# Optimization experiments

Hardware: AMD Instinct MI355X
Metric: run time of the kernel (lower is better)

Reference implementation:

```python
import jax, jax.numpy as jnp
import numpy as np

B, N_L, C, NH = 8, 256, 256, 8
HH, WW = 64, 64
N_C = HH * WW
L = 3  # focal_level
KS = [3, 5, 7]  # focal kernel sizes: focal_factor*k + focal_window
HD = C // NH
SCALE = HD ** -0.5


def _dwconv(x, w, k):
    # x: [B,C,H,W], w: [C,1,k,k] depthwise (groups=C)
    p = k // 2
    return jax.lax.conv_general_dilated(
        x, w, window_strides=(1, 1), padding=[(p, p), (p, p)],
        feature_group_count=C,
        dimension_numbers=('NCHW', 'OIHW', 'NCHW'))


def setup_inputs() -> dict:
    key = jax.random.key(0)
    ks = jax.random.split(key, 16)
    s = 0.02
    inp = {
        'latents': jax.random.normal(ks[0], (B, N_L, C), jnp.float32),
        'context': jax.random.normal(ks[1], (B, N_C, C), jnp.float32),
        'q_w': jax.random.normal(ks[2], (C, C), jnp.float32) * s,
        'k_w': jax.random.normal(ks[3], (C, C), jnp.float32) * s,
        'f_w': jax.random.normal(ks[4], (C + L + 1, C), jnp.float32) * s,
        'f_b': jnp.zeros((C + L + 1,), jnp.float32),
        'h_w': jax.random.normal(ks[5], (C, C), jnp.float32) * s,
        'h_b': jnp.zeros((C,), jnp.float32),
        'fk0': jax.random.normal(ks[6], (C, 1, KS[0], KS[0]), jnp.float32) * s,
        'fk1': jax.random.normal(ks[7], (C, 1, KS[1], KS[1]), jnp.float32) * s,
        'fk2': jax.random.normal(ks[8], (C, 1, KS[2], KS[2]), jnp.float32) * s,
        'proj_w': jax.random.normal(ks[9], (C, C), jnp.float32) * s,
        'proj_b': jnp.zeros((C,), jnp.float32),
        'H': HH,
        'W': WW,
    }
    return inp


def reference(latents, context, q_w, k_w, f_w, f_b, h_w, h_b,
              fk0, fk1, fk2, proj_w, proj_b, H, W):
    gelu = lambda x: jax.nn.gelu(x, approximate=False)
    # attention scores
    q = (latents @ q_w.T).reshape(B, N_L, NH, HD).transpose(0, 2, 1, 3)  # [B,NH,Nl,HD]
    k = (context @ k_w.T).reshape(B, N_C, NH, HD).transpose(0, 2, 1, 3)  # [B,NH,Nc,HD]
    attn = jax.nn.softmax(jnp.einsum('bhnd,bhmd->bhnm', q, k) * SCALE, axis=-1)
    # focal modulation on context
    f_out = context.reshape(B, H, W, C) @ f_w.T + f_b          # [B,H,W,C+L+1]
    f_out = f_out.transpose(0, 3, 1, 2)                        # [B,C+L+1,H,W]
    v_ctx, gates = f_out[:, :C], f_out[:, C:]
    v_ctx_all = jnp.zeros_like(v_ctx)
    for l, fk in enumerate((fk0, fk1, fk2)):
        v_ctx = gelu(_dwconv(v_ctx, fk, KS[l]))
        v_ctx_all = v_ctx_all + v_ctx * gates[:, l:l + 1]
    v_global = gelu(v_ctx.mean(axis=(2, 3), keepdims=True))
    v_ctx_all = v_ctx_all + v_global * gates[:, L:L + 1]
    # 1x1 conv modulator
    v_mod = jnp.einsum('bchw,dc->bdhw', v_ctx_all, h_w) + h_b[None, :, None, None]
    # NOTE: faithful to original -- raw reshape of NCHW tensor (no permute)
    v = v_mod.reshape(B, N_C, NH, HD).transpose(0, 2, 1, 3)    # [B,NH,Nc,HD]
    out = jnp.einsum('bhnm,bhmd->bhnd', attn, v)               # [B,NH,Nl,HD]
    out = out.transpose(0, 2, 1, 3).reshape(B, N_L, C)
    out = out @ proj_w.T + proj_b
    return out, attn
```

## Files before the change

### kernel.cpp

```cpp
#include <hip/hip_runtime.h>
#include <math.h>


namespace {

constexpr float CSCALE = 0.17677669529663688f;

typedef __attribute__((ext_vector_type(8))) __bf16 bf16x8;
typedef __attribute__((ext_vector_type(4))) float f32x4;

__device__ __forceinline__ float gelu_f(float x) {
  return 0.5f * x * (1.0f + erff(x * 0.70710678118654752f));
}

__device__ __forceinline__ unsigned short f2bf(float f) {
  union { float f; unsigned u; } v; v.f = f;
  unsigned r = v.u + 0x7fffu + ((v.u >> 16) & 1u);
  return (unsigned short)(r >> 16);
}

__device__ __forceinline__ float bf2f(unsigned short u) {
  union { unsigned u; float f; } v; v.u = (unsigned)u << 16;
  return v.f;
}

__global__ __launch_bounds__(256) void cast_all(
    const float* __restrict__ ctx, const float* __restrict__ lat,
    const float* __restrict__ qw, const float* __restrict__ kw,
    const float* __restrict__ fw, const float* __restrict__ hww,
    const float* __restrict__ pw,
    unsigned short* ctxb, unsigned short* latb, unsigned short* qwb,
    unsigned short* kwb, unsigned short* fwb, unsigned short* hwb,
    unsigned short* pwb) {
  const int blk = blockIdx.x;
  const float* s; unsigned short* d; int b0, nq;
  if      (blk < 2048) { s = ctx; d = ctxb; b0 = blk;        nq = 2097152; }
  else if (blk < 2176) { s = lat; d = latb; b0 = blk - 2048; nq = 131072; }
  else if (blk < 2192) { s = qw;  d = qwb;  b0 = blk - 2176; nq = 16384; }
  else if (blk < 2208) { s = kw;  d = kwb;  b0 = blk - 2192; nq = 16384; }
  else if (blk < 2225) { s = fw;  d = fwb;  b0 = blk - 2208; nq = 16640; }
  else if (blk < 2241) { s = hww; d = hwb;  b0 = blk - 2225; nq = 16384; }
  else                 { s = pw;  d = pwb;  b0 = blk - 2241; nq = 16384; }
  #pragma unroll
  for (int t = 0; t < 4; ++t) {
    const int q = b0*1024 + t*256 + threadIdx.x;
    if (q < nq) {
      float4 v = ((const float4*)s)[q];
      ushort4 o;
      o.x = f2bf(v.x); o.y = f2bf(v.y); o.z = f2bf(v.z); o.w = f2bf(v.w);
      ((ushort4*)d)[q] = o;
    }
  }
}

__global__ __launch_bounds__(256) void mfma_qk(
    const unsigned short* __restrict__ A, const unsigned short* __restrict__ W,
    unsigned short* __restrict__ out) {
  const int r0 = blockIdx.x * 64, n0 = blockIdx.y * 64;
  const int tid = threadIdx.x, w = tid >> 6, l = tid & 63;
  const int lr = l & 15, lk = l >> 4;
  const int rw = r0 + w*16;
  const unsigned short* ap = A + (size_t)(rw + lr)*256 + lk*8;
  f32x4 acc[4] = {{0.f,0.f,0.f,0.f},{0.f,0.f,0.f,0.f},{0.f,0.f,0.f,0.f},{0.f,0.f,0.f,0.f}};
  #pragma unroll
  for (int k0 = 0; k0 < 256; k0 += 32) {
    bf16x8 a = *reinterpret_cast<const bf16x8*>(ap + k0);
    #pragma unroll
    for (int j = 0; j < 4; ++j) {
      bf16x8 b = *reinterpret_cast<const bf16x8*>(W + (size_t)(n0 + j*16 + lr)*256 + k0 + lk*8);
      acc[j] = __builtin_amdgcn_mfma_f32_16x16x32_bf16(a, b, acc[j], 0, 0, 0);
    }
  }
  #pragma unroll
  for (int j = 0; j < 4; ++j)
    #pragma unroll
    for (int rr = 0; rr < 4; ++rr)
      out[(size_t)(rw + lk*4 + rr)*256 + n0 + j*16 + lr] = f2bf(acc[j][rr]);
}

__global__ __launch_bounds__(256) void mfma_fk(
    const unsigned short* __restrict__ A, const unsigned short* __restrict__ Wk,
    const unsigned short* __restrict__ Wf, const float* __restrict__ fb,
    unsigned short* __restrict__ kout, unsigned short* __restrict__ vctx,
    float* __restrict__ gates) {
  const int r0 = blockIdx.x * 64;
  const bool isk = blockIdx.y < 4;
  const int n0 = (isk ? blockIdx.y : blockIdx.y - 4) * 64;
  const unsigned short* W = isk ? Wk : Wf;
  const int tid = threadIdx.x, w = tid >> 6, l = tid & 63;
  const int lr = l & 15, lk = l >> 4;
  const int rw = r0 + w*16;
  const unsigned short* ap = A + (size_t)(rw + lr)*256 + lk*8;
  f32x4 acc[4] = {{0.f,0.f,0.f,0.f},{0.f,0.f,0.f,0.f},{0.f,0.f,0.f,0.f},{0.f,0.f,0.f,0.f}};
  #pragma unroll
  for (int k0 = 0; k0 < 256; k0 += 32) {
    bf16x8 a = *reinterpret_cast<const bf16x8*>(ap + k0);
    #pragma unroll
    for (int j = 0; j < 4; ++j) {
      const int n = n0 + j*16 + lr;
      bf16x8 b = {};
      if (isk || n < 260)
        b = *reinterpret_cast<const bf16x8*>(W + (size_t)n*256 + k0 + lk*8);
      acc[j] = __builtin_amdgcn_mfma_f32_16x16x32_bf16(a, b, acc[j], 0, 0, 0);
    }
  }
  if (isk) {
    #pragma unroll
    for (int j = 0; j < 4; ++j)
      #pragma unroll
      for (int rr = 0; rr < 4; ++rr)
        kout[(size_t)(rw + lk*4 + rr)*256 + n0 + j*16 + lr] = f2bf(acc[j][rr]);
  } else {
    const int rbase = rw + lk*4;
    const int b = rbase >> 12, hw = rbase & 4095;
    #pragma unroll
    for (int j = 0; j < 4; ++j) {
      const int n = n0 + j*16 + lr;
      if (n >= 260) continue;
      const float bb = fb[n];
      if (n < 256) {
        ushort4 o;
        o.x = f2bf(acc[j][0] + bb); o.y = f2bf(acc[j][1] + bb);
        o.z = f2bf(acc[j][2] + bb); o.w = f2bf(acc[j][3] + bb);
        *(ushort4*)&vctx[((size_t)(b*256 + n))*4096 + hw] = o;
      } else {
        float4 o = make_float4(acc[j][0] + bb, acc[j][1] + bb,
                               acc[j][2] + bb, acc[j][3] + bb);
        *(float4*)&gates[((size_t)(b*4 + (n - 256)))*4096 + hw] = o;
      }
    }
  }
}

__global__ __launch_bounds__(256) void fused_conv(
    const unsigned short* in, const float* __restrict__ wk3,
    const float* __restrict__ wk5, const float* __restrict__ wk7,
    const float* __restrict__ gates, unsigned short* out) {
  constexpr int TW = 70;
  __shared__ float A[TW * TW];
  __shared__ float w3[9];
  __shared__ float w5[25];
  __shared__ float w7[49];
  __shared__ float red[4];
  const int tid = threadIdx.x;
  const int b = blockIdx.x >> 8, c = blockIdx.x & 255;
  if (tid < 9)  w3[tid] = wk3[c*9  + tid];
  else if (tid < 34) w5[tid-9]  = wk5[c*25 + tid-9];
  else if (tid < 83) w7[tid-34] = wk7[c*49 + tid-34];
  const unsigned short* ip = in + (size_t)(b*256 + c) * 4096;
  for (int idx = tid; idx < TW*TW; idx += 256) {
    const int ty = idx / TW, tx = idx - ty*TW;
    const int gy = ty - 3, gx = tx - 3;
    A[idx] = (gy >= 0 && gy < 64 && gx >= 0 && gx < 64) ? bf2f(ip[gy*64 + gx]) : 0.0f;
  }
  __syncthreads();
  const float* g0 = gates + (size_t)(b*4 + 0) * 4096;
  const float* g1 = gates + (size_t)(b*4 + 1) * 4096;
  const float* g2 = gates + (size_t)(b*4 + 2) * 4096;
  const float* g3 = gates + (size_t)(b*4 + 3) * 4096;
  float v[16], acc[16];
  #pragma unroll
  for (int ii = 0; ii < 16; ++ii) {
    const int pix = ii*256 + tid;
    const int y = pix >> 6, x = pix & 63;
    float s = 0.f;
    #pragma unroll
    for (int ky = 0; ky < 3; ++ky)
      #pragma unroll
      for (int kx = 0; kx < 3; ++kx)
        s += w3[ky*3 + kx] * A[(y+2+ky)*TW + (x+2+kx)];
    v[ii] = gelu_f(s);
    acc[ii] = v[ii] * g0[pix];
  }
  __syncthreads();
  #pragma unroll
  for (int ii = 0; ii < 16; ++ii) {
    const int pix = ii*256 + tid;
    A[((pix >> 6) + 3)*TW + (pix & 63) + 3] = v[ii];
  }
  __syncthreads();
  #pragma unroll
  for (int ii = 0; ii < 16; ++ii) {
    const int pix = ii*256 + tid;
    const int y = pix >> 6, x = pix & 63;
    float s = 0.f;
    #pragma unroll
    for (int ky = 0; ky < 5; ++ky)
      #pragma unroll
      for (int kx = 0; kx < 5; ++kx)
        s += w5[ky*5 + kx] * A[(y+1+ky)*TW + (x+1+kx)];
    v[ii] = gelu_f(s);
    acc[ii] += v[ii] * g1[pix];
  }
  __syncthreads();
  #pragma unroll
  for (int ii = 0; ii < 16; ++ii) {
    const int pix = ii*256 + tid;
    A[((pix >> 6) + 3)*TW + (pix & 63) + 3] = v[ii];
  }
  __syncthreads();
  float msum = 0.f;
  #pragma unroll
  for (int ii = 0; ii < 16; ++ii) {
    const int pix = ii*256 + tid;
    const int y = pix >> 6, x = pix & 63;
    float s = 0.f;
    #pragma unroll
    for (int ky = 0; ky < 7; ++ky)
      #pragma unroll
      for (int kx = 0; kx < 7; ++kx)
        s += w7[ky*7 + kx] * A[(y+ky)*TW + (x+kx)];
    v[ii] = gelu_f(s);
    acc[ii] += v[ii] * g2[pix];
    msum += v[ii];
  }
  #pragma unroll
  for (int off = 32; off >= 1; off >>= 1) msum += __shfl_xor(msum, off, 64);
  if ((tid & 63) == 0) red[tid >> 6] = msum;
  __syncthreads();
  const float vg = gelu_f((red[0]+red[1]+red[2]+red[3]) * (1.0f/4096.0f));
  unsigned short* vp = out + (size_t)(b*256 + c) * 4096;
  #pragma unroll
  for (int ii = 0; ii < 16; ++ii) {
    const int pix = ii*256 + tid;
    vp[pix] = f2bf(acc[ii] + vg * g3[pix]);
  }
}

__global__ __launch_bounds__(256) void mfma_h(
    const unsigned short* __restrict__ vall, const unsigned short* __restrict__ hwb,
    const float* __restrict__ hb, unsigned short* __restrict__ vlin) {
  __shared__ unsigned short Bs[64][264];
  __shared__ unsigned short Ts[64][72];
  const int hw0 = blockIdx.x * 64, d0 = blockIdx.y * 64, b = blockIdx.z;
  const int tid = threadIdx.x, w = tid >> 6, l = tid & 63;
  const int lr = l & 15, lk = l >> 4;
  const int cl = tid >> 3, hl = (tid & 7) * 8;
  #pragma unroll
  for (int c0 = 0; c0 < 256; c0 += 32) {
    const unsigned short* sp = vall + (size_t)(b*256 + c0 + cl)*4096 + hw0 + hl;
    ushort4 u0 = *(const ushort4*)sp;
    ushort4 u1 = *(const ushort4*)(sp + 4);
    Bs[hl+0][c0+cl] = u0.x; Bs[hl+1][c0+cl] = u0.y;
    Bs[hl+2][c0+cl] = u0.z; Bs[hl+3][c0+cl] = u0.w;
    Bs[hl+4][c0+cl] = u1.x; Bs[hl+5][c0+cl] = u1.y;
    Bs[hl+6][c0+cl] = u1.z; Bs[hl+7][c0+cl] = u1.w;
  }
  __syncthreads();
  const int dw = d0 + w*16;
  const unsigned short* ap = hwb + (size_t)(dw + lr)*256 + lk*8;
  f32x4 acc[4] = {{0.f,0.f,0.f,0.f},{0.f,0.f,0.f,0.f},{0.f,0.f,0.f,0.f},{0.f,0.f,0.f,0.f}};
  #pragma unroll
  for (int k0 = 0; k0 < 256; k0 += 32) {
    bf16x8 a = *reinterpret_cast<const bf16x8*>(ap + k0);
    #pragma unroll
    for (int j = 0; j < 4; ++j) {
      bf16x8 bv = *reinterpret_cast<const bf16x8*>(&Bs[j*16 + lr][k0 + lk*8]);
      acc[j] = __builtin_amdgcn_mfma_f32_16x16x32_bf16(a, bv, acc[j], 0, 0, 0);
    }
  }
  float hbv[4];
  #pragma unroll
  for (int rr = 0; rr < 4; ++rr) hbv[rr] = hb[dw + lk*4 + rr];
  #pragma unroll
  for (int j = 0; j < 4; ++j)
    #pragma unroll
    for (int rr = 0; rr < 4; ++rr)
      Ts[w*16 + lk*4 + rr][j*16 + lr] = f2bf(acc[j][rr] + hbv[rr]);
  __syncthreads();
  const int q = hw0 >> 8, dim0 = hw0 & 255;
  #pragma unroll
  for (int it = 0; it < 2; ++it) {
    const int dl = it*32 + (tid >> 3);
    const int ch = tid & 7;
    const int m = (d0 + dl)*16 + q;
    uint4 v = *(const uint4*)&Ts[dl][ch*8];
    *(uint4*)&vlin[((size_t)(b*4096 + m))*256 + dim0 + ch*8] = v;
  }
}

__global__ __launch_bounds__(256) void trans_bf(
    const unsigned short* __restrict__ vlin, unsigned short* __restrict__ vt) {
  __shared__ unsigned short T[64][72];
  const int tid = threadIdx.x;
  const int m0 = blockIdx.x * 64, d0 = blockIdx.y * 64, b = blockIdx.z;
  #pragma unroll
  for (int it = 0; it < 2; ++it) {
    const int ml = it*32 + (tid >> 3);
    const int ch = tid & 7;
    uint4 v = *(const uint4*)&vlin[((size_t)(b*4096 + m0 + ml))*256 + d0 + ch*8];
    *(uint4*)&T[ml][ch*8] = v;
  }
  __syncthreads();
  #pragma unroll
  for (int it = 0; it < 2; ++it) {
    const int dl = it*32 + (tid >> 3);
    const int ch = tid & 7;
    unsigned short tmp[8];
    #pragma unroll
    for (int k = 0; k < 8; ++k) tmp[k] = T[ch*8 + k][dl];
    *(uint4*)&vt[((size_t)(b*256 + d0 + dl))*4096 + m0 + ch*8] = *(uint4*)tmp;
  }
}

__global__ __launch_bounds__(256) void attn_pv(
    const unsigned short* __restrict__ qb, const unsigned short* __restrict__ kb,
    const unsigned short* __restrict__ vt, float* __restrict__ attn,
    unsigned short* __restrict__ aout) {
  const int blk = blockIdx.x;
  const int bh = blk & 63, nt = blk >> 6;
  const int b = bh >> 3, h = bh & 7;
  const int tid = threadIdx.x;
  const int w = tid >> 6, l = tid & 63;
  const int lr = l & 15, lk = l >> 4;
  const int n0 = nt * 16;
  __shared__ float rs[4][16];
  __shared__ unsigned short pl[4][16][40];
  __shared__ float ps[4][16][34];
  __shared__ float osum[4][16][32];
  bf16x8 aq = *reinterpret_cast<const bf16x8*>(
      qb + ((size_t)(b*256 + n0 + lr))*256 + h*32 + lk*8);
  const unsigned short* kbase = kb + (size_t)b*4096*256 + h*32 + lk*8;
  float sum[4] = {0.f, 0.f, 0.f, 0.f};
  #pragma unroll 2
  for (int mt = 0; mt < 64; ++mt) {
    const int m0 = w*1024 + mt*16;
    bf16x8 bk = *reinterpret_cast<const bf16x8*>(kbase + (size_t)(m0 + lr)*256);
    f32x4 d = __builtin_amdgcn_mfma_f32_16x16x32_bf16(aq, bk, (f32x4){0.f,0.f,0.f,0.f}, 0, 0, 0);
    #pragma unroll
    for (int r = 0; r < 4; ++r) sum[r] += __expf(d[r] * CSCALE);
  }
  #pragma unroll
  for (int r = 0; r < 4; ++r) {
    #pragma unroll
    for (int m = 1; m < 16; m <<= 1) sum[r] += __shfl_xor(sum[r], m, 64);
  }
  if (lr == 0) {
    #pragma unroll
    for (int r = 0; r < 4; ++r) rs[w][lk*4 + r] = sum[r];
  }
  __syncthreads();
  float invS[4];
  #pragma unroll
  for (int r = 0; r < 4; ++r) {
    const int rowi = lk*4 + r;
    invS[r] = 1.0f / (rs[0][rowi] + rs[1][rowi] + rs[2][rowi] + rs[3][rowi]);
  }
  float* ab = attn + ((size_t)bh*256 + n0) * 4096;
  const unsigned short* vb = vt + ((size_t)(b*256 + h*32))*4096;
  const int fr = l >> 5;
  const int fm = l & 31;
  f32x4 acc0 = {0.f,0.f,0.f,0.f}, acc1 = {0.f,0.f,0.f,0.f};
  for (int mt = 0; mt < 64; ++mt) {
    const int m0 = w*1024 + mt*16;
    bf16x8 bk = *reinterpret_cast<const bf16x8*>(kbase + (size_t)(m0 + lr)*256);
    f32x4 d = __builtin_amdgcn_mfma_f32_16x16x32_bf16(aq, bk, (f32x4){0.f,0.f,0.f,0.f}, 0, 0, 0);
    const int mo = (mt & 1) << 4;
    #pragma unroll
    for (int r = 0; r < 4; ++r) {
      const float p = __expf(d[r] * CSCALE) * invS[r];
      ps[w][lk*4 + r][mo + lr] = p;
      pl[w][lk*4 + r][mo + lr] = f2bf(p);
    }
    if (mt & 1) {
      const int mb = w*1024 + (mt - 1)*16;
      bf16x8 pa = *reinterpret_cast<const bf16x8*>(&pl[w][lr][lk*8]);
      bf16x8 bv0 = *reinterpret_cast<const bf16x8*>(vb + (size_t)lr*4096 + mb + lk*8);
      bf16x8 bv1 = *reinterpret_cast<const bf16x8*>(vb + (size_t)(16 + lr)*4096 + mb + lk*8);
      acc0 = __builtin_amdgcn_mfma_f32_16x16x32_bf16(pa, bv0, acc0, 0, 0, 0);
      acc1 = __builtin_amdgcn_mfma_f32_16x16x32_bf16(pa, bv1, acc1, 0, 0, 0);
      #pragma unroll
      for (int i = 0; i < 8; ++i) {
        const int row = i*2 + fr;
        ab[(size_t)row*4096 + mb + fm] = ps[w][row][fm];
      }
    }
  }
  #pragma unroll
  for (int r = 0; r < 4; ++r) {
    osum[w][lk*4 + r][lr]      = acc0[r];
    osum[w][lk*4 + r][16 + lr] = acc1[r];
  }
  __syncthreads();
  for (int i = tid; i < 512; i += 256) {
    const int n = i >> 5, d = i & 31;
    const float s = osum[0][n][d] + osum[1][n][d] + osum[2][n][d] + osum[3][n][d];
    aout[((size_t)(b*256 + n0 + n))*256 + h*32 + d] = f2bf(s);
  }
}

__global__ __launch_bounds__(256) void mfma_proj(
    const unsigned short* __restrict__ A, const unsigned short* __restrict__ W,
    const float* __restrict__ pb, float* __restrict__ out) {
  const int r0 = blockIdx.x * 64, n0 = blockIdx.y * 64;
  const int tid = threadIdx.x, w = tid >> 6, l = tid & 63;
  const int lr = l & 15, lk = l >> 4;
  const int rw = r0 + w*16;
  const unsigned short* ap = A + (size_t)(rw + lr)*256 + lk*8;
  f32x4 acc[4] = {{0.f,0.f,0.f,0.f},{0.f,0.f,0.f,0.f},{0.f,0.f,0.f,0.f},{0.f,0.f,0.f,0.f}};
  #pragma unroll
  for (int k0 = 0; k0 < 256; k0 += 32) {
    bf16x8 a = *reinterpret_cast<const bf16x8*>(ap + k0);
    #pragma unroll
    for (int j = 0; j < 4; ++j) {
      bf16x8 b = *reinterpret_cast<const bf16x8*>(W + (size_t)(n0 + j*16 + lr)*256 + k0 + lk*8);
      acc[j] = __builtin_amdgcn_mfma_f32_16x16x32_bf16(a, b, acc[j], 0, 0, 0);
    }
  }
  #pragma unroll
  for (int j = 0; j < 4; ++j) {
    const int n = n0 + j*16 + lr;
    const float bb = pb[n];
    #pragma unroll
    for (int rr = 0; rr < 4; ++rr)
      out[(size_t)(rw + lk*4 + rr)*256 + n] = acc[j][rr] + bb;
  }
}

}

extern "C" void kernel_launch(void* const* d_in, const int* in_sizes, int n_in,
                              void* d_out, int out_size, void* d_ws, size_t ws_size,
                              hipStream_t stream) {
  (void)in_sizes; (void)n_in; (void)out_size; (void)ws_size;
  const float* latents = (const float*)d_in[0];
  const float* context = (const float*)d_in[1];
  const float* q_w    = (const float*)d_in[2];
  const float* k_w    = (const float*)d_in[3];
  const float* f_w    = (const float*)d_in[4];
  const float* f_b    = (const float*)d_in[5];
  const float* h_w    = (const float*)d_in[6];
  const float* h_b    = (const float*)d_in[7];
  const float* fk0    = (const float*)d_in[8];
  const float* fk1    = (const float*)d_in[9];
  const float* fk2    = (const float*)d_in[10];
  const float* proj_w = (const float*)d_in[11];
  const float* proj_b = (const float*)d_in[12];

  float* out0 = (float*)d_out;
  float* attn = out0 + (size_t)8*256*256;

  char* w = (char*)d_ws;
  unsigned short* ctx_bf = (unsigned short*)(w + 0x0);
  unsigned short* vcv    = (unsigned short*)(w + 0x1000000);
  unsigned short* k_bf   = (unsigned short*)(w + 0x2100000);
  unsigned short* v_tb   = (unsigned short*)(w + 0x3100000);
  unsigned short* q_bf   = (unsigned short*)(w + 0x4100000);
  unsigned short* lat_bf = (unsigned short*)(w + 0x4200000);
  unsigned short* qw_bf  = (unsigned short*)(w + 0x4300000);
  unsigned short* kw_bf  = (unsigned short*)(w + 0x4340000);
  unsigned short* fw_bf  = (unsigned short*)(w + 0x4380000);
  unsigned short* hw_bf  = (unsigned short*)(w + 0x43C0000);
  unsigned short* pw_bf  = (unsigned short*)(w + 0x4400000);
  float*          gates  = (float*)(w + 0x4440000);
  unsigned short* aout_bf= (unsigned short*)(w + 0x44C0000);
  unsigned short* vlin_bf= (unsigned short*)(w + 0x4600000);

  cast_all<<<2257, 256, 0, stream>>>(context, latents, q_w, k_w, f_w, h_w, proj_w,
                                     ctx_bf, lat_bf, qw_bf, kw_bf, fw_bf, hw_bf, pw_bf);
  mfma_qk  <<<dim3(32, 4),  256, 0, stream>>>(lat_bf, qw_bf, q_bf);
  mfma_fk  <<<dim3(512, 9), 256, 0, stream>>>(ctx_bf, kw_bf, fw_bf, f_b, k_bf, vcv, gates);
  fused_conv<<<2048, 256, 0, stream>>>(vcv, fk0, fk1, fk2, gates, vcv);
  mfma_h   <<<dim3(64, 4, 8), 256, 0, stream>>>(vcv, hw_bf, h_b, vlin_bf);
  trans_bf <<<dim3(64, 4, 8), 256, 0, stream>>>(vlin_bf, v_tb);
  attn_pv  <<<1024, 256, 0, stream>>>(q_bf, k_bf, v_tb, attn, aout_bf);
  mfma_proj<<<dim3(32, 4), 256, 0, stream>>>(aout_bf, pw_bf, proj_b, out0);
}
```

Baseline: 342.4 us.

## Fuse activation casts into GEMMs, widen GEMM N tiles, vectorize attn stores

Removes the separate fp32→bf16 cast pass over context and latents, so the Q/K/F GEMMs now read fp32 activations directly and convert them in registers. Each GEMM block now covers the full N dimension (16 or 17 MFMA tiles), so the A rows are read once instead of once per N tile. mfma_h also computes all 256 output channels per block, reusing the transposed LDS tile. The attention-probability writeout to global memory changes from scalar to float4 stores, with the LDS row padding adjusted to keep alignment. In exchange, the large per-thread accumulator arrays raise register pressure and lower occupancy, and context is now read twice in fp32 (once by the K GEMM and once by the F GEMM).

```diff
diff --git a/kernel.cpp b/kernel.cpp
--- a/kernel.cpp
+++ b/kernel.cpp
@@ -24,23 +24,26 @@
   return v.f;
 }
 
-__global__ __launch_bounds__(256) void cast_all(
-    const float* __restrict__ ctx, const float* __restrict__ lat,
+__device__ __forceinline__ bf16x8 pack8(float4 a, float4 b) {
+  union { unsigned short u[8]; bf16x8 v; } A;
+  A.u[0] = f2bf(a.x); A.u[1] = f2bf(a.y); A.u[2] = f2bf(a.z); A.u[3] = f2bf(a.w);
+  A.u[4] = f2bf(b.x); A.u[5] = f2bf(b.y); A.u[6] = f2bf(b.z); A.u[7] = f2bf(b.w);
+  return A.v;
+}
+
+__global__ __launch_bounds__(256) void cast_w(
     const float* __restrict__ qw, const float* __restrict__ kw,
     const float* __restrict__ fw, const float* __restrict__ hww,
     const float* __restrict__ pw,
-    unsigned short* ctxb, unsigned short* latb, unsigned short* qwb,
-    unsigned short* kwb, unsigned short* fwb, unsigned short* hwb,
-    unsigned short* pwb) {
+    unsigned short* qwb, unsigned short* kwb, unsigned short* fwb,
+    unsigned short* hwb, unsigned short* pwb) {
   const int blk = blockIdx.x;
   const float* s; unsigned short* d; int b0, nq;
-  if      (blk < 2048) { s = ctx; d = ctxb; b0 = blk;        nq = 2097152; }
-  else if (blk < 2176) { s = lat; d = latb; b0 = blk - 2048; nq = 131072; }
-  else if (blk < 2192) { s = qw;  d = qwb;  b0 = blk - 2176; nq = 16384; }
-  else if (blk < 2208) { s = kw;  d = kwb;  b0 = blk - 2192; nq = 16384; }
-  else if (blk < 2225) { s = fw;  d = fwb;  b0 = blk - 2208; nq = 16640; }
-  else if (blk < 2241) { s = hww; d = hwb;  b0 = blk - 2225; nq = 16384; }
-  else                 { s = pw;  d = pwb;  b0 = blk - 2241; nq = 16384; }
+  if      (blk < 16) { s = qw;  d = qwb; b0 = blk;      nq = 16384; }
+  else if (blk < 32) { s = kw;  d = kwb; b0 = blk - 16; nq = 16384; }
+  else if (blk < 49) { s = fw;  d = fwb; b0 = blk - 32; nq = 16640; }
+  else if (blk < 65) { s = hww; d = hwb; b0 = blk - 49; nq = 16384; }
+  else               { s = pw;  d = pwb; b0 = blk - 65; nq = 16384; }
   #pragma unroll
   for (int t = 0; t < 4; ++t) {
     const int q = b0*1024 + t*256 + threadIdx.x;
@@ -53,81 +56,77 @@
   }
 }
 
-__global__ __launch_bounds__(256) void mfma_qk(
-    const unsigned short* __restrict__ A, const unsigned short* __restrict__ W,
+__global__ __launch_bounds__(256) void mfma_proj_rw(
+    const float* __restrict__ A, const unsigned short* __restrict__ W,
     unsigned short* __restrict__ out) {
-  const int r0 = blockIdx.x * 64, n0 = blockIdx.y * 64;
+  const int r0 = blockIdx.x * 64;
   const int tid = threadIdx.x, w = tid >> 6, l = tid & 63;
   const int lr = l & 15, lk = l >> 4;
   const int rw = r0 + w*16;
-  const unsigned short* ap = A + (size_t)(rw + lr)*256 + lk*8;
-  f32x4 acc[4] = {{0.f,0.f,0.f,0.f},{0.f,0.f,0.f,0.f},{0.f,0.f,0.f,0.f},{0.f,0.f,0.f,0.f}};
+  const float* ap = A + (size_t)(rw + lr)*256 + lk*8;
+  f32x4 acc[16];
+  #pragma unroll
+  for (int j = 0; j < 16; ++j) acc[j] = (f32x4){0.f,0.f,0.f,0.f};
   #pragma unroll
   for (int k0 = 0; k0 < 256; k0 += 32) {
-    bf16x8 a = *reinterpret_cast<const bf16x8*>(ap + k0);
-    #pragma unroll
-    for (int j = 0; j < 4; ++j) {
-      bf16x8 b = *reinterpret_cast<const bf16x8*>(W + (size_t)(n0 + j*16 + lr)*256 + k0 + lk*8);
+    float4 c0 = *(const float4*)(ap + k0);
+    float4 c1 = *(const float4*)(ap + k0 + 4);
+    bf16x8 a = pack8(c0, c1);
+    #pragma unroll
+    for (int j = 0; j < 16; ++j) {
+      bf16x8 b = *reinterpret_cast<const bf16x8*>(W + (size_t)(j*16 + lr)*256 + k0 + lk*8);
       acc[j] = __builtin_amdgcn_mfma_f32_16x16x32_bf16(a, b, acc[j], 0, 0, 0);
     }
   }
   #pragma unroll
-  for (int j = 0; j < 4; ++j)
+  for (int j = 0; j < 16; ++j)
     #pragma unroll
     for (int rr = 0; rr < 4; ++rr)
-      out[(size_t)(rw + lk*4 + rr)*256 + n0 + j*16 + lr] = f2bf(acc[j][rr]);
-}
-
-__global__ __launch_bounds__(256) void mfma_fk(
-    const unsigned short* __restrict__ A, const unsigned short* __restrict__ Wk,
-    const unsigned short* __restrict__ Wf, const float* __restrict__ fb,
-    unsigned short* __restrict__ kout, unsigned short* __restrict__ vctx,
+      out[(size_t)(rw + lk*4 + rr)*256 + j*16 + lr] = f2bf(acc[j][rr]);
+}
+
+__global__ __launch_bounds__(256) void mfma_f(
+    const float* __restrict__ A, const unsigned short* __restrict__ W,
+    const float* __restrict__ fb, unsigned short* __restrict__ vctx,
     float* __restrict__ gates) {
   const int r0 = blockIdx.x * 64;
-  const bool isk = blockIdx.y < 4;
-  const int n0 = (isk ? blockIdx.y : blockIdx.y - 4) * 64;
-  const unsigned short* W = isk ? Wk : Wf;
   const int tid = threadIdx.x, w = tid >> 6, l = tid & 63;
   const int lr = l & 15, lk = l >> 4;
   const int rw = r0 + w*16;
-  const unsigned short* ap = A + (size_t)(rw + lr)*256 + lk*8;
-  f32x4 acc[4] = {{0.f,0.f,0.f,0.f},{0.f,0.f,0.f,0.f},{0.f,0.f,0.f,0.f},{0.f,0.f,0.f,0.f}};
+  const float* ap = A + (size_t)(rw + lr)*256 + lk*8;
+  f32x4 acc[17];
+  #pragma unroll
+  for (int j = 0; j < 17; ++j) acc[j] = (f32x4){0.f,0.f,0.f,0.f};
   #pragma unroll
   for (int k0 = 0; k0 < 256; k0 += 32) {
-    bf16x8 a = *reinterpret_cast<const bf16x8*>(ap + k0);
-    #pragma unroll
-    for (int j = 0; j < 4; ++j) {
-      const int n = n0 + j*16 + lr;
+    float4 c0 = *(const float4*)(ap + k0);
+    float4 c1 = *(const float4*)(ap + k0 + 4);
+    bf16x8 a = pack8(c0, c1);
+    #pragma unroll
+    for (int j = 0; j < 17; ++j) {
+      const int n = j*16 + lr;
       bf16x8 b = {};
-      if (isk || n < 260)
+      if (n < 260)
         b = *reinterpret_cast<const bf16x8*>(W + (size_t)n*256 + k0 + lk*8);
       acc[j] = __builtin_amdgcn_mfma_f32_16x16x32_bf16(a, b, acc[j], 0, 0, 0);
     }
   }
-  if (isk) {
-    #pragma unroll
-    for (int j = 0; j < 4; ++j)
-      #pragma unroll
-      for (int rr = 0; rr < 4; ++rr)
-        kout[(size_t)(rw + lk*4 + rr)*256 + n0 + j*16 + lr] = f2bf(acc[j][rr]);
-  } else {
-    const int rbase = rw + lk*4;
-    const int b = rbase >> 12, hw = rbase & 4095;
-    #pragma unroll
-    for (int j = 0; j < 4; ++j) {
-      const int n = n0 + j*16 + lr;
-      if (n >= 260) continue;
-      const float bb = fb[n];
-      if (n < 256) {
-        ushort4 o;
-        o.x = f2bf(acc[j][0] + bb); o.y = f2bf(acc[j][1] + bb);
-        o.z = f2bf(acc[j][2] + bb); o.w = f2bf(acc[j][3] + bb);
-        *(ushort4*)&vctx[((size_t)(b*256 + n))*4096 + hw] = o;
-      } else {
-        float4 o = make_float4(acc[j][0] + bb, acc[j][1] + bb,
-                               acc[j][2] + bb, acc[j][3] + bb);
-        *(float4*)&gates[((size_t)(b*4 + (n - 256)))*4096 + hw] = o;
-      }
+  const int rbase = rw + lk*4;
+  const int b = rbase >> 12, hw = rbase & 4095;
+  #pragma unroll
+  for (int j = 0; j < 17; ++j) {
+    const int n = j*16 + lr;
+    if (n >= 260) continue;
+    const float bb = fb[n];
+    if (n < 256) {
+      ushort4 o;
+      o.x = f2bf(acc[j][0] + bb); o.y = f2bf(acc[j][1] + bb);
+      o.z = f2bf(acc[j][2] + bb); o.w = f2bf(acc[j][3] + bb);
+      *(ushort4*)&vctx[((size_t)(b*256 + n))*4096 + hw] = o;
+    } else {
+      float4 o = make_float4(acc[j][0] + bb, acc[j][1] + bb,
+                             acc[j][2] + bb, acc[j][3] + bb);
+      *(float4*)&gates[((size_t)(b*4 + (n - 256)))*4096 + hw] = o;
     }
   }
 }
@@ -230,9 +229,8 @@
 __global__ __launch_bounds__(256) void mfma_h(
     const unsigned short* __restrict__ vall, const unsigned short* __restrict__ hwb,
     const float* __restrict__ hb, unsigned short* __restrict__ vlin) {
-  __shared__ unsigned short Bs[64][264];
-  __shared__ unsigned short Ts[64][72];
-  const int hw0 = blockIdx.x * 64, d0 = blockIdx.y * 64, b = blockIdx.z;
+  __shared__ unsigned short sh[256 * 72];
+  const int hw0 = blockIdx.x * 64, b = blockIdx.y;
   const int tid = threadIdx.x, w = tid >> 6, l = tid & 63;
   const int lr = l & 15, lk = l >> 4;
   const int cl = tid >> 3, hl = (tid & 7) * 8;
@@ -241,40 +239,53 @@
     const unsigned short* sp = vall + (size_t)(b*256 + c0 + cl)*4096 + hw0 + hl;
     ushort4 u0 = *(const ushort4*)sp;
     ushort4 u1 = *(const ushort4*)(sp + 4);
-    Bs[hl+0][c0+cl] = u0.x; Bs[hl+1][c0+cl] = u0.y;
-    Bs[hl+2][c0+cl] = u0.z; Bs[hl+3][c0+cl] = u0.w;
-    Bs[hl+4][c0+cl] = u1.x; Bs[hl+5][c0+cl] = u1.y;
-    Bs[hl+6][c0+cl] = u1.z; Bs[hl+7][c0+cl] = u1.w;
-  }
-  __syncthreads();
-  const int dw = d0 + w*16;
-  const unsigned short* ap = hwb + (size_t)(dw + lr)*256 + lk*8;
-  f32x4 acc[4] = {{0.f,0.f,0.f,0.f},{0.f,0.f,0.f,0.f},{0.f,0.f,0.f,0.f},{0.f,0.f,0.f,0.f}};
+    sh[(hl+0)*264 + c0+cl] = u0.x; sh[(hl+1)*264 + c0+cl] = u0.y;
+    sh[(hl+2)*264 + c0+cl] = u0.z; sh[(hl+3)*264 + c0+cl] = u0.w;
+    sh[(hl+4)*264 + c0+cl] = u1.x; sh[(hl+5)*264 + c0+cl] = u1.y;
+    sh[(hl+6)*264 + c0+cl] = u1.z; sh[(hl+7)*264 + c0+cl] = u1.w;
+  }
+  __syncthreads();
+  const int dw = w * 64;
+  f32x4 acc[4][4];
+  #pragma unroll
+  for (int j2 = 0; j2 < 4; ++j2)
+    #pragma unroll
+    for (int j = 0; j < 4; ++j) acc[j2][j] = (f32x4){0.f,0.f,0.f,0.f};
   #pragma unroll
   for (int k0 = 0; k0 < 256; k0 += 32) {
-    bf16x8 a = *reinterpret_cast<const bf16x8*>(ap + k0);
+    bf16x8 a[4];
+    #pragma unroll
+    for (int j2 = 0; j2 < 4; ++j2)
+      a[j2] = *reinterpret_cast<const bf16x8*>(hwb + (size_t)(dw + j2*16 + lr)*256 + k0 + lk*8);
     #pragma unroll
     for (int j = 0; j < 4; ++j) {
-      bf16x8 bv = *reinterpret_cast<const bf16x8*>(&Bs[j*16 + lr][k0 + lk*8]);
-      acc[j] = __builtin_amdgcn_mfma_f32_16x16x32_bf16(a, bv, acc[j], 0, 0, 0);
-    }
-  }
-  float hbv[4];
-  #pragma unroll
-  for (int rr = 0; rr < 4; ++rr) hbv[rr] = hb[dw + lk*4 + rr];
-  #pragma unroll
-  for (int j = 0; j < 4; ++j)
-    #pragma unroll
-    for (int rr = 0; rr < 4; ++rr)
-      Ts[w*16 + lk*4 + rr][j*16 + lr] = f2bf(acc[j][rr] + hbv[rr]);
+      bf16x8 bv = *reinterpret_cast<const bf16x8*>(&sh[(j*16 + lr)*264 + k0 + lk*8]);
+      #pragma unroll
+      for (int j2 = 0; j2 < 4; ++j2)
+        acc[j2][j] = __builtin_amdgcn_mfma_f32_16x16x32_bf16(a[j2], bv, acc[j2][j], 0, 0, 0);
+    }
+  }
+  float hbv[4][4];
+  #pragma unroll
+  for (int j2 = 0; j2 < 4; ++j2)
+    #pragma unroll
+    for (int rr = 0; rr < 4; ++rr) hbv[j2][rr] = hb[dw + j2*16 + lk*4 + rr];
+  __syncthreads();
+  #pragma unroll
+  for (int j2 = 0; j2 < 4; ++j2)
+    #pragma unroll
+    for (int j = 0; j < 4; ++j)
+      #pragma unroll
+      for (int rr = 0; rr < 4; ++rr)
+        sh[(dw + j2*16 + lk*4 + rr)*72 + j*16 + lr] = f2bf(acc[j2][j][rr] + hbv[j2][rr]);
   __syncthreads();
   const int q = hw0 >> 8, dim0 = hw0 & 255;
   #pragma unroll
-  for (int it = 0; it < 2; ++it) {
+  for (int it = 0; it < 8; ++it) {
     const int dl = it*32 + (tid >> 3);
     const int ch = tid & 7;
-    const int m = (d0 + dl)*16 + q;
-    uint4 v = *(const uint4*)&Ts[dl][ch*8];
+    const int m = dl*16 + q;
+    uint4 v = *(const uint4*)&sh[dl*72 + ch*8];
     *(uint4*)&vlin[((size_t)(b*4096 + m))*256 + dim0 + ch*8] = v;
   }
 }
@@ -316,7 +327,7 @@
   const int n0 = nt * 16;
   __shared__ float rs[4][16];
   __shared__ unsigned short pl[4][16][40];
-  __shared__ float ps[4][16][34];
+  __shared__ float ps[4][16][36];
   __shared__ float osum[4][16][32];
   bf16x8 aq = *reinterpret_cast<const bf16x8*>(
       qb + ((size_t)(b*256 + n0 + lr))*256 + h*32 + lk*8);
@@ -348,8 +359,8 @@
   }
   float* ab = attn + ((size_t)bh*256 + n0) * 4096;
   const unsigned short* vb = vt + ((size_t)(b*256 + h*32))*4096;
-  const int fr = l >> 5;
-  const int fm = l & 31;
+  const int fr = l >> 3;
+  const int fm = (l & 7) * 4;
   f32x4 acc0 = {0.f,0.f,0.f,0.f}, acc1 = {0.f,0.f,0.f,0.f};
   for (int mt = 0; mt < 64; ++mt) {
     const int m0 = w*1024 + mt*16;
@@ -370,9 +381,10 @@
       acc0 = __builtin_amdgcn_mfma_f32_16x16x32_bf16(pa, bv0, acc0, 0, 0, 0);
       acc1 = __builtin_amdgcn_mfma_f32_16x16x32_bf16(pa, bv1, acc1, 0, 0, 0);
       #pragma unroll
-      for (int i = 0; i < 8; ++i) {
-        const int row = i*2 + fr;
-        ab[(size_t)row*4096 + mb + fm] = ps[w][row][fm];
+      for (int i = 0; i < 2; ++i) {
+        const int row = i*8 + fr;
+        float4 pv4 = *(const float4*)&ps[w][row][fm];
+        *(float4*)&ab[(size_t)row*4096 + mb + fm] = pv4;
       }
     }
   }
@@ -441,27 +453,26 @@
   float* attn = out0 + (size_t)8*256*256;
 
   char* w = (char*)d_ws;
-  unsigned short* ctx_bf = (unsigned short*)(w + 0x0);
-  unsigned short* vcv    = (unsigned short*)(w + 0x1000000);
-  unsigned short* k_bf   = (unsigned short*)(w + 0x2100000);
-  unsigned short* v_tb   = (unsigned short*)(w + 0x3100000);
-  unsigned short* q_bf   = (unsigned short*)(w + 0x4100000);
-  unsigned short* lat_bf = (unsigned short*)(w + 0x4200000);
-  unsigned short* qw_bf  = (unsigned short*)(w + 0x4300000);
-  unsigned short* kw_bf  = (unsigned short*)(w + 0x4340000);
-  unsigned short* fw_bf  = (unsigned short*)(w + 0x4380000);
-  unsigned short* hw_bf  = (unsigned short*)(w + 0x43C0000);
-  unsigned short* pw_bf  = (unsigned short*)(w + 0x4400000);
-  float*          gates  = (float*)(w + 0x4440000);
-  unsigned short* aout_bf= (unsigned short*)(w + 0x44C0000);
-  unsigned short* vlin_bf= (unsigned short*)(w + 0x4600000);
-
-  cast_all<<<2257, 256, 0, stream>>>(context, latents, q_w, k_w, f_w, h_w, proj_w,
-                                     ctx_bf, lat_bf, qw_bf, kw_bf, fw_bf, hw_bf, pw_bf);
-  mfma_qk  <<<dim3(32, 4),  256, 0, stream>>>(lat_bf, qw_bf, q_bf);
-  mfma_fk  <<<dim3(512, 9), 256, 0, stream>>>(ctx_bf, kw_bf, fw_bf, f_b, k_bf, vcv, gates);
+  unsigned short* vcv     = (unsigned short*)(w + 0x0);
+  unsigned short* k_bf    = (unsigned short*)(w + 0x1000000);
+  unsigned short* v_tb    = (unsigned short*)(w + 0x2000000);
+  unsigned short* vlin_bf = (unsigned short*)(w + 0x3000000);
+  unsigned short* q_bf    = (unsigned short*)(w + 0x4000000);
+  unsigned short* aout_bf = (unsigned short*)(w + 0x4100000);
+  unsigned short* qw_bf   = (unsigned short*)(w + 0x4200000);
+  unsigned short* kw_bf   = (unsigned short*)(w + 0x4220000);
+  unsigned short* fw_bf   = (unsigned short*)(w + 0x4240000);
+  unsigned short* hw_bf   = (unsigned short*)(w + 0x4270000);
+  unsigned short* pw_bf   = (unsigned short*)(w + 0x4290000);
+  float*          gates   = (float*)(w + 0x42B0000);
+
+  cast_w<<<81, 256, 0, stream>>>(q_w, k_w, f_w, h_w, proj_w,
+                                 qw_bf, kw_bf, fw_bf, hw_bf, pw_bf);
+  mfma_proj_rw<<<32,  256, 0, stream>>>(latents, qw_bf, q_bf);
+  mfma_proj_rw<<<512, 256, 0, stream>>>(context, kw_bf, k_bf);
+  mfma_f   <<<512, 256, 0, stream>>>(context, fw_bf, f_b, vcv, gates);
   fused_conv<<<2048, 256, 0, stream>>>(vcv, fk0, fk1, fk2, gates, vcv);
-  mfma_h   <<<dim3(64, 4, 8), 256, 0, stream>>>(vcv, hw_bf, h_b, vlin_bf);
+  mfma_h   <<<dim3(64, 8), 256, 0, stream>>>(vcv, hw_bf, h_b, vlin_bf);
   trans_bf <<<dim3(64, 4, 8), 256, 0, stream>>>(vlin_bf, v_tb);
   attn_pv  <<<1024, 256, 0, stream>>>(q_bf, k_bf, v_tb, attn, aout_bf);
   mfma_proj<<<dim3(32, 4), 256, 0, stream>>>(aout_bf, pw_bf, proj_b, out0);
```

After: 350.1 us. 2.2% more time.
